# Optimization experiments

Hardware: AMD Instinct MI355X
Metric: run time of the kernel (lower is better)

Reference implementation:

```python
import jax, jax.numpy as jnp
import numpy as np

N_NODES = 20000
N_EDGES = 320000
IN_C = 128
H0, H1 = 256, 256
OUT_C = 64


def _glorot(key, shape):
    lim = float(np.sqrt(6.0 / (shape[0] + shape[1])))
    return jax.random.uniform(key, shape, jnp.float32, -lim, lim)


def setup_inputs() -> dict:
    key = jax.random.key(0)
    ks = jax.random.split(key, 16)
    x = jax.random.normal(ks[0], (N_NODES, IN_C), jnp.float32)
    edge_index = jax.random.randint(ks[1], (2, N_EDGES), 0, N_NODES, jnp.int64)
    return {
        "x": x,
        "edge_index": edge_index,
        # conv1: in -> h0
        "W1l": _glorot(ks[2], (IN_C, H0)), "b1": jnp.zeros((H0,), jnp.float32), "W1r": _glorot(ks[3], (IN_C, H0)),
        # conv_list[0]: h0 -> h1
        "W2l": _glorot(ks[4], (H0, H1)), "b2": jnp.zeros((H1,), jnp.float32), "W2r": _glorot(ks[5], (H0, H1)),
        # initial residual: in -> h1
        "Wres": _glorot(ks[6], (IN_C, H1)), "bres": jnp.zeros((H1,), jnp.float32),
        # conv_mu: h1 -> out
        "Wmul": _glorot(ks[7], (H1, OUT_C)), "bmu": jnp.zeros((OUT_C,), jnp.float32), "Wmur": _glorot(ks[8], (H1, OUT_C)),
        # conv_logstd: h1 -> out
        "Wlsl": _glorot(ks[9], (H1, OUT_C)), "bls": jnp.zeros((OUT_C,), jnp.float32), "Wlsr": _glorot(ks[10], (H1, OUT_C)),
    }


def _sage(x, src, dst, Wl, b, Wr):
    """PyG SAGEConv with mean aggregation: lin_l(mean_j x_j) + lin_r(x_i)."""
    n = x.shape[0]
    msgs = x[src]                                             # [E, d] gather
    s = jax.ops.segment_sum(msgs, dst, num_segments=n)        # [N, d]
    deg = jax.ops.segment_sum(jnp.ones((src.shape[0],), x.dtype), dst, num_segments=n)
    agg = s / jnp.maximum(deg, 1.0)[:, None]
    return agg @ Wl + b + x @ Wr


def reference(x, edge_index, W1l, b1, W1r, W2l, b2, W2r, Wres, bres,
              Wmul, bmu, Wmur, Wlsl, bls, Wlsr):
    src, dst = edge_index[0], edge_index[1]
    h = jax.nn.relu(_sage(x, src, dst, W1l, b1, W1r))
    h = jax.nn.relu(_sage(h, src, dst, W2l, b2, W2r)) + (x @ Wres + bres)
    mu = _sage(h, src, dst, Wmul, bmu, Wmur)
    logstd = _sage(h, src, dst, Wlsl, bls, Wlsr)
    return mu, logstd
```

## Files before the change

kernel.cpp:

```cpp
#include <hip/hip_runtime.h>
#include <cstddef>

#define NN 20000
#define NE 320000

typedef short bf16x8 __attribute__((ext_vector_type(8)));
typedef float f32x4 __attribute__((ext_vector_type(4)));
typedef unsigned short u16;

__device__ __forceinline__ float bf2f(u16 u) {
    unsigned x = ((unsigned)u) << 16;
    return __builtin_bit_cast(float, x);
}
__device__ __forceinline__ u16 f2bf(float f) {
    unsigned x = __builtin_bit_cast(unsigned, f);
    x = (x + 0x7fff + ((x >> 16) & 1)) >> 16;
    return (u16)x;
}

__global__ __launch_bounds__(256) void detect_kernel(const void* __restrict__ edges, int* flag) {
    __shared__ int bad;
    if (threadIdx.x == 0) bad = 0;
    __syncthreads();
    int any = 0;
    for (int i = blockIdx.x * 256 + threadIdx.x; i < NE; i += 64 * 256) {
        long long v = ((const long long*)edges)[i];
        if (v < 0 || v >= NN) any = 1;
    }
    if (any) bad = 1;
    __syncthreads();
    if (threadIdx.x == 0 && bad) atomicOr(flag, 1);
}

__global__ __launch_bounds__(256) void convert_kernel(const void* __restrict__ edges,
                                                      const int* __restrict__ flag,
                                                      int* __restrict__ src, int* __restrict__ dst,
                                                      int* __restrict__ deg) {
    int i = blockIdx.x * blockDim.x + threadIdx.x;
    if (i >= NE) return;
    int s, d;
    if (*flag) {
        s = ((const int*)edges)[i];
        d = ((const int*)edges)[NE + i];
    } else {
        s = (int)((const long long*)edges)[i];
        d = (int)((const long long*)edges)[NE + i];
    }
    src[i] = s;
    dst[i] = d;
    atomicAdd(&deg[d], 1);
}

__global__ __launch_bounds__(256) void scan1_kernel(const int* __restrict__ deg,
                                                    int* __restrict__ incl, int* __restrict__ bsum) {
    __shared__ int buf[256];
    int t = threadIdx.x, i = blockIdx.x * 256 + t;
    int v = (i < NN) ? deg[i] : 0;
    buf[t] = v;
    __syncthreads();
    for (int off = 1; off < 256; off <<= 1) {
        int u = (t >= off) ? buf[t - off] : 0;
        __syncthreads();
        buf[t] += u;
        __syncthreads();
    }
    if (i < NN) incl[i] = buf[t];
    if (t == 255) bsum[blockIdx.x] = buf[255];
}

__global__ __launch_bounds__(256) void scan2_kernel(const int* __restrict__ bsum,
                                                    int* __restrict__ boff) {
    __shared__ int buf[256];
    const int nb = (NN + 255) / 256;
    int t = threadIdx.x;
    int v = (t < nb) ? bsum[t] : 0;
    buf[t] = v;
    __syncthreads();
    for (int off = 1; off < 256; off <<= 1) {
        int u = (t >= off) ? buf[t - off] : 0;
        __syncthreads();
        buf[t] += u;
        __syncthreads();
    }
    if (t < nb) boff[t] = buf[t] - v;
}

__global__ __launch_bounds__(256) void scan3_kernel(const int* __restrict__ deg,
                                                    const int* __restrict__ incl,
                                                    const int* __restrict__ boff,
                                                    int* __restrict__ rowptr) {
    int i = blockIdx.x * 256 + threadIdx.x;
    if (i < NN) rowptr[i] = boff[i >> 8] + incl[i] - deg[i];
    if (i == NN) rowptr[NN] = NE;
}

__global__ __launch_bounds__(256) void fill_kernel(const int* __restrict__ src,
                                                   const int* __restrict__ dst,
                                                   const int* __restrict__ rowptr,
                                                   int* __restrict__ cursor,
                                                   int* __restrict__ csr_src) {
    int i = blockIdx.x * blockDim.x + threadIdx.x;
    if (i >= NE) return;
    int d = dst[i];
    int p = atomicAdd(&cursor[d], 1);
    csr_src[rowptr[d] + p] = src[i];
}

__global__ __launch_bounds__(256) void cast_kernel(const float* __restrict__ in,
                                                   u16* __restrict__ out, int n4) {
    int i = blockIdx.x * 256 + threadIdx.x;
    if (i >= n4) return;
    float4 v = *(const float4*)(in + (size_t)i * 4);
    ushort4 o;
    o.x = f2bf(v.x); o.y = f2bf(v.y); o.z = f2bf(v.z); o.w = f2bf(v.w);
    *(ushort4*)(out + (size_t)i * 4) = o;
}

struct WJobs {
    const float* W[9];
    u16* WT[9];
    int K[9];
    int N[9];
};
__global__ __launch_bounds__(256) void wtrans_all(WJobs jobs) {
    int y = blockIdx.y;
    int K = jobs.K[y], N = jobs.N[y];
    int i = blockIdx.x * 256 + threadIdx.x;
    if (i >= K * N) return;
    int k = i / N, n = i % N;
    jobs.WT[y][(size_t)n * K + k] = f2bf(jobs.W[y][i]);
}

template <int D>
__global__ __launch_bounds__(256) void aggregate_kernel(const u16* __restrict__ feat,
                                                        const int* __restrict__ csr_src,
                                                        const int* __restrict__ rowptr,
                                                        u16* __restrict__ out) {
    int node = blockIdx.x * 4 + (threadIdx.x >> 6);
    if (node >= NN) return;
    int lane = threadIdx.x & 63;
    int beg = rowptr[node], end = rowptr[node + 1];
    int cnt = end - beg;
    float inv = 1.0f / (float)(cnt > 0 ? cnt : 1);

    constexpr int NSUB = (D == 256) ? 2 : 4;
    constexpr int LPG = 64 / NSUB;
    int sub = lane / LPG;
    int c8 = lane % LPG;
    const u16* fc = feat + c8 * 8;

    float a0[8] = {0.f,0.f,0.f,0.f,0.f,0.f,0.f,0.f};
    float a1[8] = {0.f,0.f,0.f,0.f,0.f,0.f,0.f,0.f};

    int e = beg + sub;
    for (; e + 3 * NSUB < end; e += 4 * NSUB) {
        int s0 = csr_src[e];
        int s1 = csr_src[e + NSUB];
        int s2 = csr_src[e + 2 * NSUB];
        int s3 = csr_src[e + 3 * NSUB];
        bf16x8 u0 = *(const bf16x8*)(fc + (size_t)s0 * D);
        bf16x8 u1 = *(const bf16x8*)(fc + (size_t)s1 * D);
        bf16x8 u2 = *(const bf16x8*)(fc + (size_t)s2 * D);
        bf16x8 u3 = *(const bf16x8*)(fc + (size_t)s3 * D);
#pragma unroll
        for (int j = 0; j < 8; j++) {
            a0[j] += bf2f((u16)u0[j]) + bf2f((u16)u2[j]);
            a1[j] += bf2f((u16)u1[j]) + bf2f((u16)u3[j]);
        }
    }
    for (; e < end; e += NSUB) {
        int s = csr_src[e];
        bf16x8 u = *(const bf16x8*)(fc + (size_t)s * D);
#pragma unroll
        for (int j = 0; j < 8; j++) a0[j] += bf2f((u16)u[j]);
    }
#pragma unroll
    for (int j = 0; j < 8; j++) {
        a0[j] += a1[j];
        if (NSUB == 4) a0[j] += __shfl_xor(a0[j], 16);
        a0[j] += __shfl_xor(a0[j], 32);
    }
    if (sub == 0) {
        bf16x8 o;
#pragma unroll
        for (int j = 0; j < 8; j++) o[j] = (short)f2bf(a0[j] * inv);
        *(bf16x8*)(out + (size_t)node * D + c8 * 8) = o;
    }
}

__global__ __launch_bounds__(256) void agg_final(const u16* __restrict__ R,
                                                 const int* __restrict__ csr_src,
                                                 const int* __restrict__ rowptr,
                                                 const float* __restrict__ bmu,
                                                 const float* __restrict__ bls,
                                                 float* __restrict__ out) {
    int node = blockIdx.x * 4 + (threadIdx.x >> 6);
    if (node >= NN) return;
    int lane = threadIdx.x & 63;
    int beg = rowptr[node], end = rowptr[node + 1];
    int cnt = end - beg;
    float inv = 1.0f / (float)(cnt > 0 ? cnt : 1);

    int sub = lane >> 4;
    int c8 = lane & 15;
    const u16* fc = R + c8 * 8;

    float a0[8] = {0.f,0.f,0.f,0.f,0.f,0.f,0.f,0.f};
    float a1[8] = {0.f,0.f,0.f,0.f,0.f,0.f,0.f,0.f};

    int e = beg + sub;
    for (; e + 12 < end; e += 16) {
        int s0 = csr_src[e];
        int s1 = csr_src[e + 4];
        int s2 = csr_src[e + 8];
        int s3 = csr_src[e + 12];
        bf16x8 u0 = *(const bf16x8*)(fc + (size_t)s0 * 256);
        bf16x8 u1 = *(const bf16x8*)(fc + (size_t)s1 * 256);
        bf16x8 u2 = *(const bf16x8*)(fc + (size_t)s2 * 256);
        bf16x8 u3 = *(const bf16x8*)(fc + (size_t)s3 * 256);
#pragma unroll
        for (int j = 0; j < 8; j++) {
            a0[j] += bf2f((u16)u0[j]) + bf2f((u16)u2[j]);
            a1[j] += bf2f((u16)u1[j]) + bf2f((u16)u3[j]);
        }
    }
    for (; e < end; e += 4) {
        int s = csr_src[e];
        bf16x8 u = *(const bf16x8*)(fc + (size_t)s * 256);
#pragma unroll
        for (int j = 0; j < 8; j++) a0[j] += bf2f((u16)u[j]);
    }
#pragma unroll
    for (int j = 0; j < 8; j++) {
        a0[j] += a1[j];
        a0[j] += __shfl_xor(a0[j], 16);
        a0[j] += __shfl_xor(a0[j], 32);
    }
    if (sub == 0) {
        int c0 = c8 * 8;
        bf16x8 q = *(const bf16x8*)(R + (size_t)node * 256 + 128 + c0);
        float o[8];
#pragma unroll
        for (int j = 0; j < 8; j++) {
            int c = c0 + j;
            float b = (c < 64) ? bmu[c] : bls[c - 64];
            o[j] = a0[j] * inv + bf2f((u16)q[j]) + b;
        }
        float* dst = (c0 < 64) ? (out + (size_t)node * 64 + c0)
                               : (out + (size_t)NN * 64 + (size_t)node * 64 + (c0 - 64));
        *(float4*)dst = make_float4(o[0], o[1], o[2], o[3]);
        *(float4*)(dst + 4) = make_float4(o[4], o[5], o[6], o[7]);
    }
}

template <int KS0, int KS1, int KS2, int RELU01, int OUT_F32, int NWAVES>
__global__ __launch_bounds__(NWAVES * 64) void gemm_lds(
    const u16* __restrict__ A0, const u16* __restrict__ B0T,
    const u16* __restrict__ A1, const u16* __restrict__ B1T,
    const u16* __restrict__ A2, const u16* __restrict__ B2T,
    const float* __restrict__ bias, const float* __restrict__ bias2,
    void* __restrict__ Cout, int M) {
    constexpr int NT = NWAVES * 64;
    constexpr int NCOL = NWAVES * 64;
    constexpr int AI = 4096 / (NT * 16);
    constexpr int BI = (NCOL * 64) / (NT * 16);
    constexpr int TOT = KS0 + KS1 + KS2;
    constexpr int pS1 = KS0, pS2 = KS0 + KS1;
    constexpr int BOFF = 64 * 32;
    constexpr int BUFSZ = BOFF + NCOL * 32;

    __shared__ __align__(16) u16 smem[2][BUFSZ];

    const int t = threadIdx.x;
    const int w = t >> 6, l = t & 63;
    const int l15 = l & 15, lhi = l >> 4;
    const int rowBase = blockIdx.x * 64;
    const int wc = w * 64;
    const int srow = t >> 2, skk = t & 3;

    f32x4 acc[4][4];
#pragma unroll
    for (int r = 0; r < 4; r++)
#pragma unroll
        for (int n = 0; n < 4; n++) acc[r][n] = f32x4{0.f, 0.f, 0.f, 0.f};

    bf16x8 ar[AI], br[BI];

    auto gload = [&](const u16* __restrict__ A, const u16* __restrict__ BT, int K, int ko) {
#pragma unroll
        for (int i = 0; i < AI; i++) {
            int row = rowBase + i * (NT / 4) + srow;
            row = row < M ? row : M - 1;
            ar[i] = *(const bf16x8*)(A + (size_t)row * K + ko + skk * 8);
        }
#pragma unroll
        for (int i = 0; i < BI; i++) {
            int n = i * (NT / 4) + srow;
            br[i] = *(const bf16x8*)(BT + (size_t)n * K + ko + skk * 8);
        }
    };
    auto swrite = [&](int buf) {
        u16* base = smem[buf];
#pragma unroll
        for (int i = 0; i < AI; i++)
            *(bf16x8*)(base + (size_t)(i * NT + t) * 8) = ar[i];
#pragma unroll
        for (int i = 0; i < BI; i++)
            *(bf16x8*)(base + BOFF + (size_t)(i * NT + t) * 8) = br[i];
    };

    gload(A0, B0T, KS0 * 32, 0);
    int cur = 0;

#pragma unroll 1
    for (int step = 0; step < TOT; step++) {
        __syncthreads();
        swrite(cur);
        int ns = step + 1;
        if (ns < TOT) {
            if (KS2 > 0 && ns >= pS2)       gload(A2, B2T, KS2 * 32, (ns - pS2) * 32);
            else if (KS1 > 0 && ns >= pS1)  gload(A1, B1T, KS1 * 32, (ns - pS1) * 32);
            else                            gload(A0, B0T, KS0 * 32, ns * 32);
        }
        __syncthreads();
        const u16* sb = smem[cur];
        bf16x8 af[4], bf[4];
#pragma unroll
        for (int r = 0; r < 4; r++)
            af[r] = *(const bf16x8*)(sb + (r * 16 + l15) * 32 + lhi * 8);
#pragma unroll
        for (int n = 0; n < 4; n++)
            bf[n] = *(const bf16x8*)(sb + BOFF + (wc + n * 16 + l15) * 32 + lhi * 8);
#pragma unroll
        for (int r = 0; r < 4; r++)
#pragma unroll
            for (int n = 0; n < 4; n++)
                acc[r][n] = __builtin_amdgcn_mfma_f32_16x16x32_bf16(af[r], bf[n], acc[r][n], 0, 0, 0);
        if (RELU01 && step == pS2 - 1) {
#pragma unroll
            for (int n = 0; n < 4; n++) {
                float b = bias[wc + n * 16 + l15];
#pragma unroll
                for (int r = 0; r < 4; r++)
#pragma unroll
                    for (int j = 0; j < 4; j++)
                        acc[r][n][j] = fmaxf(acc[r][n][j] + b, 0.f);
            }
        }
        cur ^= 1;
    }

#pragma unroll
    for (int n = 0; n < 4; n++) {
        int col = wc + n * 16 + l15;
        float badd;
        if constexpr (KS2 > 0)      badd = bias2[col];
        else if constexpr (RELU01)  badd = 0.f;
        else                        badd = bias[col];
#pragma unroll
        for (int r = 0; r < 4; r++) {
#pragma unroll
            for (int j = 0; j < 4; j++) {
                int row = rowBase + r * 16 + lhi * 4 + j;
                if (row >= M) continue;
                float v = acc[r][n][j] + badd;
                if constexpr (OUT_F32) {
                    ((float*)Cout)[(size_t)row * NCOL + col] = v;
                } else {
                    ((u16*)Cout)[(size_t)row * NCOL + col] = f2bf(v);
                }
            }
        }
    }
}

extern "C" void kernel_launch(void* const* d_in, const int* in_sizes, int n_in,
                              void* d_out, int out_size, void* d_ws, size_t ws_size,
                              hipStream_t stream) {
    const float* x    = (const float*)d_in[0];
    const void*  edges = d_in[1];
    const float* W1l  = (const float*)d_in[2];
    const float* b1   = (const float*)d_in[3];
    const float* W1r  = (const float*)d_in[4];
    const float* W2l  = (const float*)d_in[5];
    const float* b2   = (const float*)d_in[6];
    const float* W2r  = (const float*)d_in[7];
    const float* Wres = (const float*)d_in[8];
    const float* bres = (const float*)d_in[9];
    const float* Wmul = (const float*)d_in[10];
    const float* bmu  = (const float*)d_in[11];
    const float* Wmur = (const float*)d_in[12];
    const float* Wlsl = (const float*)d_in[13];
    const float* bls  = (const float*)d_in[14];
    const float* Wlsr = (const float*)d_in[15];
    float* out = (float*)d_out;

    char* ws = (char*)d_ws;
    size_t off = 0;
    int*   flag   = (int*)(ws + off); off += 256;
    int*   deg    = (int*)(ws + off); off += (size_t)NN * 4;
    int*   cursor = (int*)(ws + off); off += (size_t)NN * 4;
    float* zerosf = (float*)(ws + off); off += 1024;
    const size_t zlen = off;
    int* src     = (int*)(ws + off); off += (size_t)NE * 4;
    int* dst     = (int*)(ws + off); off += (size_t)NE * 4;
    int* csr_src = (int*)(ws + off); off += (size_t)NE * 4;
    int* rowptr  = (int*)(ws + off); off += (size_t)(NN + 8) * 4;
    int* incl    = (int*)(ws + off); off += (size_t)NN * 4;
    int* bsum    = (int*)(ws + off); off += 256 * 4;
    int* boff    = (int*)(ws + off); off += 256 * 4;
    off = (off + 255) & ~(size_t)255;
    u16* xb    = (u16*)(ws + off); off += (size_t)NN * 128 * 2;
    u16* agg1b = (u16*)(ws + off); off += (size_t)NN * 128 * 2;
    u16* h1b   = (u16*)(ws + off); off += (size_t)NN * 256 * 2;
    u16* h2b   = (u16*)(ws + off); off += (size_t)NN * 256 * 2;
    u16* aggb  = (u16*)(ws + off); off += (size_t)NN * 256 * 2;
    u16* Rb    = (u16*)(ws + off); off += (size_t)NN * 256 * 2;
    u16* W1lT  = (u16*)(ws + off); off += 128 * 256 * 2;
    u16* W1rT  = (u16*)(ws + off); off += 128 * 256 * 2;
    u16* W2lT  = (u16*)(ws + off); off += 256 * 256 * 2;
    u16* W2rT  = (u16*)(ws + off); off += 256 * 256 * 2;
    u16* WresT = (u16*)(ws + off); off += 128 * 256 * 2;
    u16* Wcat  = (u16*)(ws + off); off += 256 * 256 * 2;

    hipMemsetAsync(flag, 0, zlen, stream);

    const int SB = (NN + 255) / 256;

    detect_kernel<<<64, 256, 0, stream>>>(edges, flag);
    convert_kernel<<<NE / 256, 256, 0, stream>>>(edges, flag, src, dst, deg);
    scan1_kernel<<<SB, 256, 0, stream>>>(deg, incl, bsum);
    scan2_kernel<<<1, 256, 0, stream>>>(bsum, boff);
    scan3_kernel<<<SB, 256, 0, stream>>>(deg, incl, boff, rowptr);
    fill_kernel<<<NE / 256, 256, 0, stream>>>(src, dst, rowptr, cursor, csr_src);

    cast_kernel<<<(NN * 128 / 4 + 255) / 256, 256, 0, stream>>>(x, xb, NN * 128 / 4);

    WJobs jobs;
    jobs.W[0] = W1l;  jobs.WT[0] = W1lT;           jobs.K[0] = 128; jobs.N[0] = 256;
    jobs.W[1] = W1r;  jobs.WT[1] = W1rT;           jobs.K[1] = 128; jobs.N[1] = 256;
    jobs.W[2] = W2l;  jobs.WT[2] = W2lT;           jobs.K[2] = 256; jobs.N[2] = 256;
    jobs.W[3] = W2r;  jobs.WT[3] = W2rT;           jobs.K[3] = 256; jobs.N[3] = 256;
    jobs.W[4] = Wres; jobs.WT[4] = WresT;          jobs.K[4] = 128; jobs.N[4] = 256;
    jobs.W[5] = Wmul; jobs.WT[5] = Wcat;           jobs.K[5] = 256; jobs.N[5] = 64;
    jobs.W[6] = Wlsl; jobs.WT[6] = Wcat + 64*256;  jobs.K[6] = 256; jobs.N[6] = 64;
    jobs.W[7] = Wmur; jobs.WT[7] = Wcat + 128*256; jobs.K[7] = 256; jobs.N[7] = 64;
    jobs.W[8] = Wlsr; jobs.WT[8] = Wcat + 192*256; jobs.K[8] = 256; jobs.N[8] = 64;
    wtrans_all<<<dim3(256, 9), 256, 0, stream>>>(jobs);

    const int GB = (NN + 63) / 64;

    aggregate_kernel<128><<<NN / 4, 256, 0, stream>>>(xb, csr_src, rowptr, agg1b);
    gemm_lds<4, 4, 0, 1, 0, 4><<<GB, 256, 0, stream>>>(
        agg1b, W1lT, xb, W1rT, nullptr, nullptr, b1, nullptr, h1b, NN);

    aggregate_kernel<256><<<NN / 4, 256, 0, stream>>>(h1b, csr_src, rowptr, aggb);
    gemm_lds<8, 8, 4, 1, 0, 4><<<GB, 256, 0, stream>>>(
        aggb, W2lT, h1b, W2rT, xb, WresT, b2, bres, h2b, NN);

    gemm_lds<8, 0, 0, 0, 0, 4><<<GB, 256, 0, stream>>>(
        h2b, Wcat, nullptr, nullptr, nullptr, nullptr, zerosf, nullptr, Rb, NN);
    agg_final<<<NN / 4, 256, 0, stream>>>(Rb, csr_src, rowptr, bmu, bls, out);
}
```

Before: 173.2 us.

## Merge scan kernels, fold x cast into weight transpose, deepen aggregate unroll

Fuses the second and third scan passes into one kernel in which each block reduces the preceding block sums itself. Folds the x fp32-to-bf16 cast into the weight-transpose launch as an extra grid-stride job. Raises the aggregate gather unroll to 8 for D=256 so more gathers are in flight. Together this removes two launches and adds memory-level parallelism, at the cost of redundant per-block reductions and higher register use in the aggregate kernel.

```diff
diff --git a/kernel.cpp b/kernel.cpp
--- a/kernel.cpp
+++ b/kernel.cpp
@@ -68,29 +68,21 @@
     if (t == 255) bsum[blockIdx.x] = buf[255];
 }
 
-__global__ __launch_bounds__(256) void scan2_kernel(const int* __restrict__ bsum,
-                                                    int* __restrict__ boff) {
-    __shared__ int buf[256];
-    const int nb = (NN + 255) / 256;
-    int t = threadIdx.x;
-    int v = (t < nb) ? bsum[t] : 0;
-    buf[t] = v;
+__global__ __launch_bounds__(256) void scan23_kernel(const int* __restrict__ deg,
+                                                     const int* __restrict__ incl,
+                                                     const int* __restrict__ bsum,
+                                                     int* __restrict__ rowptr) {
+    __shared__ int red[256];
+    int b = blockIdx.x, t = threadIdx.x;
+    red[t] = (t < b) ? bsum[t] : 0;
     __syncthreads();
-    for (int off = 1; off < 256; off <<= 1) {
-        int u = (t >= off) ? buf[t - off] : 0;
+    for (int off = 128; off > 0; off >>= 1) {
+        if (t < off) red[t] += red[t + off];
         __syncthreads();
-        buf[t] += u;
-        __syncthreads();
-    }
-    if (t < nb) boff[t] = buf[t] - v;
-}
-
-__global__ __launch_bounds__(256) void scan3_kernel(const int* __restrict__ deg,
-                                                    const int* __restrict__ incl,
-                                                    const int* __restrict__ boff,
-                                                    int* __restrict__ rowptr) {
-    int i = blockIdx.x * 256 + threadIdx.x;
-    if (i < NN) rowptr[i] = boff[i >> 8] + incl[i] - deg[i];
+    }
+    int boff = red[0];
+    int i = b * 256 + t;
+    if (i < NN) rowptr[i] = boff + incl[i] - deg[i];
     if (i == NN) rowptr[NN] = NE;
 }
 
@@ -106,29 +98,30 @@
     csr_src[rowptr[d] + p] = src[i];
 }
 
-__global__ __launch_bounds__(256) void cast_kernel(const float* __restrict__ in,
-                                                   u16* __restrict__ out, int n4) {
-    int i = blockIdx.x * 256 + threadIdx.x;
-    if (i >= n4) return;
-    float4 v = *(const float4*)(in + (size_t)i * 4);
-    ushort4 o;
-    o.x = f2bf(v.x); o.y = f2bf(v.y); o.z = f2bf(v.z); o.w = f2bf(v.w);
-    *(ushort4*)(out + (size_t)i * 4) = o;
-}
-
 struct WJobs {
-    const float* W[9];
-    u16* WT[9];
-    int K[9];
-    int N[9];
+    const float* W[10];
+    u16* WT[10];
+    int K[10];
+    int N[10];
 };
 __global__ __launch_bounds__(256) void wtrans_all(WJobs jobs) {
     int y = blockIdx.y;
     int K = jobs.K[y], N = jobs.N[y];
-    int i = blockIdx.x * 256 + threadIdx.x;
-    if (i >= K * N) return;
-    int k = i / N, n = i % N;
-    jobs.WT[y][(size_t)n * K + k] = f2bf(jobs.W[y][i]);
+    if (K == 0) {
+        const float* in = jobs.W[y];
+        u16* o = jobs.WT[y];
+        for (int i = blockIdx.x * 256 + threadIdx.x; i < N; i += gridDim.x * 256) {
+            float4 v = *(const float4*)(in + (size_t)i * 4);
+            ushort4 u;
+            u.x = f2bf(v.x); u.y = f2bf(v.y); u.z = f2bf(v.z); u.w = f2bf(v.w);
+            *(ushort4*)(o + (size_t)i * 4) = u;
+        }
+        return;
+    }
+    for (int i = blockIdx.x * 256 + threadIdx.x; i < K * N; i += gridDim.x * 256) {
+        int k = i / N, n = i % N;
+        jobs.WT[y][(size_t)n * K + k] = f2bf(jobs.W[y][i]);
+    }
 }
 
 template <int D>
@@ -144,6 +137,7 @@
     float inv = 1.0f / (float)(cnt > 0 ? cnt : 1);
 
     constexpr int NSUB = (D == 256) ? 2 : 4;
+    constexpr int UNR = (D == 256) ? 8 : 4;
     constexpr int LPG = 64 / NSUB;
     int sub = lane / LPG;
     int c8 = lane % LPG;
@@ -153,19 +147,20 @@
     float a1[8] = {0.f,0.f,0.f,0.f,0.f,0.f,0.f,0.f};
 
     int e = beg + sub;
-    for (; e + 3 * NSUB < end; e += 4 * NSUB) {
-        int s0 = csr_src[e];
-        int s1 = csr_src[e + NSUB];
-        int s2 = csr_src[e + 2 * NSUB];
-        int s3 = csr_src[e + 3 * NSUB];
-        bf16x8 u0 = *(const bf16x8*)(fc + (size_t)s0 * D);
-        bf16x8 u1 = *(const bf16x8*)(fc + (size_t)s1 * D);
-        bf16x8 u2 = *(const bf16x8*)(fc + (size_t)s2 * D);
-        bf16x8 u3 = *(const bf16x8*)(fc + (size_t)s3 * D);
-#pragma unroll
-        for (int j = 0; j < 8; j++) {
-            a0[j] += bf2f((u16)u0[j]) + bf2f((u16)u2[j]);
-            a1[j] += bf2f((u16)u1[j]) + bf2f((u16)u3[j]);
+    for (; e + (UNR - 1) * NSUB < end; e += UNR * NSUB) {
+        int s[UNR];
+#pragma unroll
+        for (int q = 0; q < UNR; q++) s[q] = csr_src[e + q * NSUB];
+        bf16x8 u[UNR];
+#pragma unroll
+        for (int q = 0; q < UNR; q++) u[q] = *(const bf16x8*)(fc + (size_t)s[q] * D);
+#pragma unroll
+        for (int q = 0; q < UNR; q += 2) {
+#pragma unroll
+            for (int j = 0; j < 8; j++) {
+                a0[j] += bf2f((u16)u[q][j]);
+                a1[j] += bf2f((u16)u[q + 1][j]);
+            }
         }
     }
     for (; e < end; e += NSUB) {
@@ -408,7 +403,6 @@
     int* rowptr  = (int*)(ws + off); off += (size_t)(NN + 8) * 4;
     int* incl    = (int*)(ws + off); off += (size_t)NN * 4;
     int* bsum    = (int*)(ws + off); off += 256 * 4;
-    int* boff    = (int*)(ws + off); off += 256 * 4;
     off = (off + 255) & ~(size_t)255;
     u16* xb    = (u16*)(ws + off); off += (size_t)NN * 128 * 2;
     u16* agg1b = (u16*)(ws + off); off += (size_t)NN * 128 * 2;
@@ -430,11 +424,8 @@
     detect_kernel<<<64, 256, 0, stream>>>(edges, flag);
     convert_kernel<<<NE / 256, 256, 0, stream>>>(edges, flag, src, dst, deg);
     scan1_kernel<<<SB, 256, 0, stream>>>(deg, incl, bsum);
-    scan2_kernel<<<1, 256, 0, stream>>>(bsum, boff);
-    scan3_kernel<<<SB, 256, 0, stream>>>(deg, incl, boff, rowptr);
+    scan23_kernel<<<SB, 256, 0, stream>>>(deg, incl, bsum, rowptr);
     fill_kernel<<<NE / 256, 256, 0, stream>>>(src, dst, rowptr, cursor, csr_src);
-
-    cast_kernel<<<(NN * 128 / 4 + 255) / 256, 256, 0, stream>>>(x, xb, NN * 128 / 4);
 
     WJobs jobs;
     jobs.W[0] = W1l;  jobs.WT[0] = W1lT;           jobs.K[0] = 128; jobs.N[0] = 256;
@@ -446,7 +437,8 @@
     jobs.W[6] = Wlsl; jobs.WT[6] = Wcat + 64*256;  jobs.K[6] = 256; jobs.N[6] = 64;
     jobs.W[7] = Wmur; jobs.WT[7] = Wcat + 128*256; jobs.K[7] = 256; jobs.N[7] = 64;
     jobs.W[8] = Wlsr; jobs.WT[8] = Wcat + 192*256; jobs.K[8] = 256; jobs.N[8] = 64;
-    wtrans_all<<<dim3(256, 9), 256, 0, stream>>>(jobs);
+    jobs.W[9] = x;    jobs.WT[9] = xb;             jobs.K[9] = 0;   jobs.N[9] = NN * 128 / 4;
+    wtrans_all<<<dim3(640, 10), 256, 0, stream>>>(jobs);
 
     const int GB = (NN + 63) / 64;
 
```

After: 174.1 us. About the same (+0.5%).
